# Performance work log

Measured on AMD Instinct MI355X. Metric: run time of the kernel, lower is better.

The kernel has to match this reference:

```python
import jax, jax.numpy as jnp
import numpy as np

B, S, N, F = 4, 8, 1024, 6
H, L, K, D = 64, 3, 16, 3  # hidden, layers, neighbors, num_dims
EPS = 1e-6


def setup_inputs() -> dict:
    key = jax.random.key(0)
    ks = iter(jax.random.split(key, 64))

    def w(shape, fan_in):
        return jax.random.normal(next(ks), shape, jnp.float32) / np.sqrt(fan_in)

    inp = {
        'points': jax.random.normal(next(ks), (B, S, N, F), jnp.float32),
        'w_in': w((F, H), F), 'b_in': jnp.zeros((H,), jnp.float32),
        # stacked per-layer params for the 3 PointTransformerLayers
        'Wq': w((L, H, H), H), 'bq': jnp.zeros((L, H), jnp.float32),
        'Wk': w((L, H, H), H), 'bk': jnp.zeros((L, H), jnp.float32),
        'Wv': w((L, H, H), H), 'bv': jnp.zeros((L, H), jnp.float32),
        'Wpe': w((L, D, H), D), 'bpe': jnp.zeros((L, H), jnp.float32),
        'Wpd': w((L, D, H), D), 'bpd': jnp.zeros((L, H), jnp.float32),
        'Wa': w((L, H, 1), H), 'ba': jnp.zeros((L, 1), jnp.float32),
        'Wo': w((L, H, H), H), 'bo': jnp.zeros((L, H), jnp.float32),
        'ln_s': jnp.ones((L, H), jnp.float32), 'ln_b': jnp.zeros((L, H), jnp.float32),
        # EncoderTransformerLayer params
        'Wek': w((H, H), H), 'bek': jnp.zeros((H,), jnp.float32),
        'Weq': w((H, H), H), 'beq': jnp.zeros((H,), jnp.float32),
        'Wev': w((H, H), H), 'bev': jnp.zeros((H,), jnp.float32),
        'We1': w((H, H), H), 'be1': jnp.zeros((H,), jnp.float32),
        'We2': w((H, H), H), 'be2': jnp.zeros((H,), jnp.float32),
        'ln2_s': jnp.ones((H,), jnp.float32), 'ln2_b': jnp.zeros((H,), jnp.float32),
    }
    return inp


def _layernorm(x, scale, bias):
    mu = jnp.mean(x, axis=-1, keepdims=True)
    var = jnp.var(x, axis=-1, keepdims=True)
    return (x - mu) * jax.lax.rsqrt(var + EPS) * scale + bias


def _point_layer(x, pos, Wq, bq, Wk, bk, Wv, bv, Wpe, bpe, Wpd, bpd, Wa, ba, Wo, bo):
    # x: [B,S,N,H], pos: [B,S,N,3]
    q = x @ Wq + bq
    k = x @ Wk + bk
    v = x @ Wv + bv
    pos_enc = pos @ Wpe + bpe  # [B,S,N,H]
    # pairwise squared distances: diff[i,j] = pos[i] - pos[j]
    pos_diff = pos[..., :, None, :] - pos[..., None, :, :]  # [B,S,N,N,3]
    dist = jnp.sum(pos_diff ** 2, axis=-1)                  # [B,S,N,N]
    _, nidx = jax.lax.top_k(-dist, K)                       # [B,S,N,K]

    def gather(a):  # a: [B,S,N,C] -> [B,S,N,K,C]
        return jnp.take_along_axis(a[:, :, None], nidx[..., None], axis=3)

    k_n = gather(k)
    v_n = gather(v)
    p_n = gather(pos_enc)
    qp = (q + pos_enc)[..., None, :]                        # [B,S,N,1,H]
    pd_enc = (gather(pos) - pos[..., None, :]) @ Wpd + bpd  # [B,S,N,K,H]
    scale = jnp.sqrt(jnp.float32(H))
    attn = qp * (k_n + p_n + pd_enc) / scale                # [B,S,N,K,H]
    attn = (attn @ Wa + ba).squeeze(-1)                     # [B,S,N,K]
    attn = jax.nn.softmax(attn, axis=-1)
    out = jnp.sum(attn[..., None] * v_n, axis=-2)           # [B,S,N,H]
    out = jax.nn.gelu(out @ Wo + bo)
    return x + out


def _encoder_layer(x, Wek, bek, Weq, beq, Wev, bev, We1, be1, We2, be2):
    k = x @ Wek + bek
    q = x @ Weq + beq
    v = x @ Wev + bev
    aw = jnp.einsum('bth,bsh->bts', q, k)
    aw = jax.nn.softmax(aw / jnp.sqrt(jnp.float32(H)), axis=-1)
    out = jnp.einsum('bts,bsh->bth', aw, v)
    out = jax.nn.gelu(out @ We1 + be1) @ We2 + be2
    return x + out


def reference(points, w_in, b_in, Wq, bq, Wk, bk, Wv, bv, Wpe, bpe, Wpd, bpd,
              Wa, ba, Wo, bo, ln_s, ln_b, Wek, bek, Weq, beq, Wev, bev,
              We1, be1, We2, be2, ln2_s, ln2_b):
    pos = points[..., :D]
    x = points @ w_in + b_in
    for i in range(L):
        x = _point_layer(x, pos, Wq[i], bq[i], Wk[i], bk[i], Wv[i], bv[i],
                         Wpe[i], bpe[i], Wpd[i], bpd[i], Wa[i], ba[i], Wo[i], bo[i])
        x = _layernorm(x, ln_s[i], ln_b[i])
    x = jnp.max(x, axis=-2)  # pool over points -> [B,S,H]
    x = _encoder_layer(x, Wek, bek, Weq, beq, Wev, bev, We1, be1, We2, be2)
    x = _layernorm(x, ln2_s, ln2_b)
    x = jnp.max(x, axis=-2)  # pool over seq -> [B,H]
    return x
```

## Files before the change

kernel.cpp:

```cpp
#include <hip/hip_runtime.h>
#include <cfloat>
#include <cmath>
#include <cstdint>

#define NPT   1024
#define NCL   32
#define PTOT  32768
#define HH    64
#define KNN_K 16
#define KNN_BLKS (NCL * 256)

#define RFL(x) __builtin_amdgcn_readfirstlane(x)

__device__ __forceinline__ float wave_sum64(float t) {
#pragma unroll
  for (int o = 32; o > 0; o >>= 1) t += __shfl_xor(t, o, 64);
  return t;
}

template <int NV>
__device__ __forceinline__ float mreduce(const float (&P)[NV], int lane) {
  float buf[NV];
#pragma unroll
  for (int i = 0; i < NV; ++i) buf[i] = P[i];
#pragma unroll
  for (int s = 0; (1 << s) < NV; ++s) {
    bool hi = (lane & (1 << s)) != 0;
#pragma unroll
    for (int m = 0; m < (NV >> (s + 1)); ++m) {
      float a = buf[2 * m], b = buf[2 * m + 1];
      float keep = hi ? b : a;
      float send = hi ? a : b;
      buf[m] = keep + __shfl_xor(send, 1 << s, 64);
    }
  }
  float t = buf[0];
#pragma unroll
  for (int o = NV; o < 64; o <<= 1) t += __shfl_xor(t, o, 64);
  return t;
}

__device__ __forceinline__ float gelu_f(float z) {
  float zc = 0.7978845608028654f * (z + 0.044715f * z * z * z);
  float t = __expf(2.0f * zc);
  float th = 1.0f - 2.0f / (t + 1.0f);
  return 0.5f * z * (1.0f + th);
}

__global__ __launch_bounds__(256) void k_front(
    const float* __restrict__ pts, const float* __restrict__ w_in,
    const float* __restrict__ b_in, float* __restrict__ x,
    float* __restrict__ pos4, int* __restrict__ nidx) {
  if (blockIdx.x >= KNN_BLKS) {
    int p = (blockIdx.x - KNN_BLKS) * 4 + (threadIdx.x >> 6);
    int h = threadIdx.x & 63;
    const float* pp = pts + p * 6;
    float acc = b_in[h];
#pragma unroll
    for (int f = 0; f < 6; ++f) acc += pp[f] * w_in[f * HH + h];
    x[p * HH + h] = acc;
    if (h < 4) pos4[p * 4 + h] = (h < 3) ? pp[h] : 0.0f;
    return;
  }

  __shared__ float sx[NPT], sy[NPT], sz[NPT];
  int cloud = blockIdx.x >> 8;
  int qbase = (blockIdx.x & 255) * 4;
  const float* cp = pts + (size_t)cloud * NPT * 6;
  for (int j = threadIdx.x; j < NPT; j += 256) {
    sx[j] = cp[j * 6 + 0];
    sy[j] = cp[j * 6 + 1];
    sz[j] = cp[j * 6 + 2];
  }
  __syncthreads();

  int wv = threadIdx.x >> 6;
  int lane = threadIdx.x & 63;
  int i = qbase + wv;
  float qx = sx[i], qy = sy[i], qz = sz[i];

  unsigned du[16];
#pragma unroll
  for (int c = 0; c < 16; ++c) {
    int j = c * 64 + lane;
    float dx = qx - sx[j], dy = qy - sy[j], dz = qz - sz[j];
    float d2 = __fadd_rn(__fadd_rn(__fmul_rn(dx, dx), __fmul_rn(dy, dy)),
                         __fmul_rn(dz, dz));
    du[c] = __float_as_uint(d2);
  }

  unsigned t = 0u;
#pragma unroll
  for (int bit = 30; bit >= 15; --bit) {
    unsigned tp = t | (1u << bit);
    int cnt = 0;
#pragma unroll
    for (int c = 0; c < 16; ++c)
      cnt += __popcll(__ballot(du[c] < tp));
    if (cnt <= 15) t = tp;
  }

  int obase = (cloud * NPT + i) * KNN_K;
  unsigned long long below = (1ull << lane) - 1ull;
  int slot = 0;
#pragma unroll
  for (int c = 0; c < 16; ++c) {
    bool lt = du[c] < t;
    unsigned long long m = __ballot(lt);
    if (lt) {
      int off = __popcll(m & below);
      nidx[obase + slot + off] = c * 64 + lane;
    }
    slot += __popcll(m);
  }

  int erem = KNN_K - slot;
  unsigned hi_end = t + (1u << 15);
  unsigned bu[16];
#pragma unroll
  for (int c = 0; c < 16; ++c)
    bu[c] = (du[c] >= t && du[c] < hi_end) ? du[c] : 0xFFFFFFFFu;
  for (int r2 = 0; r2 < erem; ++r2) {
    unsigned bd = bu[0];
    int bc = 0;
#pragma unroll
    for (int c = 1; c < 16; ++c) {
      if (bu[c] < bd) { bd = bu[c]; bc = c; }
    }
    unsigned gd = bd;
#pragma unroll
    for (int o = 32; o > 0; o >>= 1) {
      unsigned g2 = (unsigned)__shfl_xor((int)gd, o, 64);
      gd = (g2 < gd) ? g2 : gd;
    }
    int myidx = bc * 64 + lane;
    int gidx = (bd == gd) ? myidx : 0x7fffffff;
#pragma unroll
    for (int o = 32; o > 0; o >>= 1) {
      int g2 = __shfl_xor(gidx, o, 64);
      gidx = (g2 < gidx) ? g2 : gidx;
    }
    if (lane == 0) nidx[obase + slot + r2] = gidx;
    int sel = (myidx == gidx) ? bc : 99;
#pragma unroll
    for (int c = 0; c < 16; ++c) bu[c] = (c == sel) ? 0xFFFFFFFFu : bu[c];
  }
}

__global__ __launch_bounds__(256) void k_qkv_gemm(
    const float* __restrict__ x, const float* __restrict__ pos4,
    const float* __restrict__ Wq, const float* __restrict__ bq,
    const float* __restrict__ Wk, const float* __restrict__ bk,
    const float* __restrict__ Wv, const float* __restrict__ bv,
    const float* __restrict__ Wpe, const float* __restrict__ bpe,
    const float* __restrict__ Wpd, const float* __restrict__ bpd,
    float* __restrict__ qq, float* __restrict__ kkv) {
  int lane = threadIdx.x & 63;
  int pb = RFL(blockIdx.x * 16 + (threadIdx.x >> 6) * 4);
  const float* xw = x + (size_t)pb * HH;
  const float4* posw = reinterpret_cast<const float4*>(pos4) + pb;

  float wpe0 = Wpe[lane], wpe1 = Wpe[HH + lane], wpe2 = Wpe[2 * HH + lane];
  float wpd0 = Wpd[lane], wpd1 = Wpd[HH + lane], wpd2 = Wpd[2 * HH + lane];
  float we0 = wpe0 + wpd0, we1 = wpe1 + wpd1, we2 = wpe2 + wpd2;
  float bqq = bq[lane] + bpe[lane];
  float bkk = bk[lane] + bpe[lane] + bpd[lane];
  float bvv = bv[lane];

  float aq[4], ak[4], av[4];
#pragma unroll
  for (int p = 0; p < 4; ++p) { aq[p] = bqq; ak[p] = bkk; av[p] = bvv; }

#pragma unroll
  for (int c = 0; c < 8; ++c) {
    float wq8[8], wk8[8], wv8[8];
#pragma unroll
    for (int j = 0; j < 8; ++j) {
      int g = c * 8 + j;
      wq8[j] = Wq[g * HH + lane];
      wk8[j] = Wk[g * HH + lane];
      wv8[j] = Wv[g * HH + lane];
    }
#pragma unroll
    for (int p = 0; p < 4; ++p) {
#pragma unroll
      for (int j = 0; j < 8; ++j) {
        float xv = xw[p * HH + c * 8 + j];
        aq[p] = fmaf(xv, wq8[j], aq[p]);
        ak[p] = fmaf(xv, wk8[j], ak[p]);
        av[p] = fmaf(xv, wv8[j], av[p]);
      }
    }
  }

#pragma unroll
  for (int p = 0; p < 4; ++p) {
    float4 pp = posw[p];
    float qv = aq[p] + pp.x * wpe0 + pp.y * wpe1 + pp.z * wpe2;
    float kv = ak[p] + pp.x * we0 + pp.y * we1 + pp.z * we2;
    qq[(size_t)(pb + p) * HH + lane] = qv;
    reinterpret_cast<float2*>(kkv + ((size_t)(pb + p) << 7))[lane] =
        make_float2(kv, av[p]);
  }
}

__global__ __launch_bounds__(256) void k_attn_core(
    float* __restrict__ qq, const float* __restrict__ kkv,
    const int* __restrict__ nidx, const float* __restrict__ pos4,
    const float* __restrict__ Wpd, const float* __restrict__ Wa,
    const float* __restrict__ ba) {
  int lane = threadIdx.x & 63;
  int bid = blockIdx.x;
  int vb = (bid & 7) * (PTOT / 4 / 8) + (bid >> 3);
  int pu = RFL(vb * 4 + (threadIdx.x >> 6));
  int cbase = pu & ~(NPT - 1);

  float4 pp = reinterpret_cast<const float4*>(pos4)[pu];
  float u = qq[(size_t)pu * HH + lane] * Wa[lane] * 0.125f;
  float pdq = pp.x * Wpd[lane] + pp.y * Wpd[HH + lane] + pp.z * Wpd[2 * HH + lane];
  float C0 = wave_sum64(u * pdq) - ba[0];

  const int4* niw = reinterpret_cast<const int4*>(nidx + (size_t)pu * KNN_K);
  int nj[KNN_K];
#pragma unroll
  for (int g = 0; g < 4; ++g) {
    int4 r = niw[g];
    nj[g * 4 + 0] = r.x; nj[g * 4 + 1] = r.y;
    nj[g * 4 + 2] = r.z; nj[g * 4 + 3] = r.w;
  }

  float vj[KNN_K], P[KNN_K];
#pragma unroll
  for (int jj = 0; jj < KNN_K; ++jj) {
    float2 kv = reinterpret_cast<const float2*>(
        kkv + ((size_t)(cbase + nj[jj]) << 7))[lane];
    vj[jj] = kv.y;
    P[jj] = u * kv.x;
  }

  float T = mreduce<16>(P, lane);
  float lg = T - C0;

  float mx = lg;
#pragma unroll
  for (int o = 1; o < 16; o <<= 1) mx = fmaxf(mx, __shfl_xor(mx, o, 64));
  float e = __expf(lg - mx);
  float s = e;
#pragma unroll
  for (int o = 1; o < 16; o <<= 1) s += __shfl_xor(s, o, 64);

  float oacc = 0.f;
  int sb = lane & 48;
#pragma unroll
  for (int jj = 0; jj < KNN_K; ++jj)
    oacc = fmaf(__shfl(e, sb | jj, 64), vj[jj], oacc);

  qq[(size_t)pu * HH + lane] = oacc / s;
}

__global__ __launch_bounds__(256) void k_wo_ln(
    const float* __restrict__ outb, const float* __restrict__ Wo,
    const float* __restrict__ bo, float* __restrict__ x,
    const float* __restrict__ ln_s, const float* __restrict__ ln_b,
    float* __restrict__ partial, int do_pool) {
  __shared__ float red[4][HH];
  int lane = threadIdx.x & 63;
  int wv = threadIdx.x >> 6;
  int pb = RFL(blockIdx.x * 16 + wv * 4);
  const float* ow = outb + (size_t)pb * HH;

  float acc[4];
  float b0 = bo[lane];
#pragma unroll
  for (int p = 0; p < 4; ++p) acc[p] = b0;

#pragma unroll
  for (int c = 0; c < 8; ++c) {
    float w8[8];
#pragma unroll
    for (int j = 0; j < 8; ++j) w8[j] = Wo[(c * 8 + j) * HH + lane];
#pragma unroll
    for (int p = 0; p < 4; ++p) {
#pragma unroll
      for (int j = 0; j < 8; ++j) {
        float ov = ow[p * HH + c * 8 + j];
        acc[p] = fmaf(ov, w8[j], acc[p]);
      }
    }
  }

  float sg = ln_s[lane], bg = ln_b[lane];
  float xn[4];
#pragma unroll
  for (int p = 0; p < 4; ++p)
    xn[p] = x[(size_t)(pb + p) * HH + lane] + gelu_f(acc[p]);

  float Ts = mreduce<4>(xn, lane);
  float dd[4], sq[4];
#pragma unroll
  for (int p = 0; p < 4; ++p) {
    float mu = __shfl(Ts, p, 64) * (1.0f / HH);
    dd[p] = xn[p] - mu;
    sq[p] = dd[p] * dd[p];
  }
  float Tv = mreduce<4>(sq, lane);
  float mxp = -FLT_MAX;
#pragma unroll
  for (int p = 0; p < 4; ++p) {
    float var = __shfl(Tv, p, 64) * (1.0f / HH);
    float yv = dd[p] * rsqrtf(var + 1e-6f) * sg + bg;
    x[(size_t)(pb + p) * HH + lane] = yv;
    mxp = fmaxf(mxp, yv);
  }

  if (do_pool) {
    red[wv][lane] = mxp;
    __syncthreads();
    if (wv == 0) {
      float m = fmaxf(fmaxf(red[0][lane], red[1][lane]),
                      fmaxf(red[2][lane], red[3][lane]));
      partial[(size_t)blockIdx.x * HH + lane] = m;
    }
  }
}

__global__ __launch_bounds__(512) void k_enc(
    const float* __restrict__ partial,
    const float* __restrict__ Wek, const float* __restrict__ bek,
    const float* __restrict__ Weq, const float* __restrict__ beq,
    const float* __restrict__ Wev, const float* __restrict__ bev,
    const float* __restrict__ We1, const float* __restrict__ be1,
    const float* __restrict__ We2, const float* __restrict__ be2,
    const float* __restrict__ ln2_s, const float* __restrict__ ln2_b,
    float* __restrict__ out) {
  __shared__ float xs[8][HH], ks[8][HH], vs[8][HH], x2[8][HH];
  int b = blockIdx.x;
  int t = threadIdx.x >> 6;
  int h = threadIdx.x & 63;
  {
    int ci = b * 8 + t;
    const float* pp = partial + (size_t)ci * 64 * HH + h;
    float mx = pp[0];
#pragma unroll
    for (int c8 = 1; c8 < 64; ++c8) mx = fmaxf(mx, pp[c8 * HH]);
    xs[t][h] = mx;
  }
  __syncthreads();

  float kk = bek[h], qq = beq[h], vv = bev[h];
#pragma unroll 8
  for (int g = 0; g < HH; ++g) {
    float xv = xs[t][g];
    kk += xv * Wek[g * HH + h];
    qq += xv * Weq[g * HH + h];
    vv += xv * Wev[g * HH + h];
  }
  ks[t][h] = kk;
  vs[t][h] = vv;
  __syncthreads();

  float logit[8];
#pragma unroll
  for (int s = 0; s < 8; ++s) {
    float tt = qq * ks[s][h];
    logit[s] = wave_sum64(tt) * 0.125f;
  }
  float m = logit[0];
#pragma unroll
  for (int s = 1; s < 8; ++s) m = fmaxf(m, logit[s]);
  float ssum = 0.f;
#pragma unroll
  for (int s = 0; s < 8; ++s) { logit[s] = expf(logit[s] - m); ssum += logit[s]; }
  float o = 0.f;
#pragma unroll
  for (int s = 0; s < 8; ++s) o += (logit[s] / ssum) * vs[s][h];

  float h1 = be1[h];
#pragma unroll 8
  for (int g = 0; g < HH; ++g) h1 += __shfl(o, g, 64) * We1[g * HH + h];
  h1 = gelu_f(h1);
  float h2 = be2[h];
#pragma unroll 8
  for (int g = 0; g < HH; ++g) h2 += __shfl(h1, g, 64) * We2[g * HH + h];

  float xn = xs[t][h] + h2;
  float mu = wave_sum64(xn) * (1.0f / HH);
  float d = xn - mu;
  float var = wave_sum64(d * d) * (1.0f / HH);
  float yv = d * rsqrtf(var + 1e-6f) * ln2_s[h] + ln2_b[h];
  x2[t][h] = yv;
  __syncthreads();
  if (t == 0) {
    float mm = x2[0][h];
#pragma unroll
    for (int s = 1; s < 8; ++s) mm = fmaxf(mm, x2[s][h]);
    out[b * HH + h] = mm;
  }
}

extern "C" void kernel_launch(void* const* d_in, const int* in_sizes, int n_in,
                              void* d_out, int out_size, void* d_ws, size_t ws_size,
                              hipStream_t stream) {
  const float* points = (const float*)d_in[0];
  const float* w_in   = (const float*)d_in[1];
  const float* b_in   = (const float*)d_in[2];
  const float* Wq     = (const float*)d_in[3];
  const float* bq     = (const float*)d_in[4];
  const float* Wk     = (const float*)d_in[5];
  const float* bk     = (const float*)d_in[6];
  const float* Wv     = (const float*)d_in[7];
  const float* bv     = (const float*)d_in[8];
  const float* Wpe    = (const float*)d_in[9];
  const float* bpe    = (const float*)d_in[10];
  const float* Wpd    = (const float*)d_in[11];
  const float* bpd    = (const float*)d_in[12];
  const float* Wa     = (const float*)d_in[13];
  const float* ba     = (const float*)d_in[14];
  const float* Wo     = (const float*)d_in[15];
  const float* bo     = (const float*)d_in[16];
  const float* ln_s   = (const float*)d_in[17];
  const float* ln_b   = (const float*)d_in[18];
  const float* Wek    = (const float*)d_in[19];
  const float* bek    = (const float*)d_in[20];
  const float* Weq    = (const float*)d_in[21];
  const float* beq    = (const float*)d_in[22];
  const float* Wev    = (const float*)d_in[23];
  const float* bev    = (const float*)d_in[24];
  const float* We1    = (const float*)d_in[25];
  const float* be1    = (const float*)d_in[26];
  const float* We2    = (const float*)d_in[27];
  const float* be2    = (const float*)d_in[28];
  const float* ln2_s  = (const float*)d_in[29];
  const float* ln2_b  = (const float*)d_in[30];

  float* ws      = (float*)d_ws;
  float* pos4    = ws;
  float* xbuf    = pos4 + 4 * PTOT;
  float* qbuf    = xbuf + 64 * PTOT;
  float* kkv     = qbuf + 64 * PTOT;
  float* partial = kkv + 128 * PTOT;
  int*   nidx    = (int*)(partial + 2048 * HH);

  k_front<<<KNN_BLKS + PTOT / 4, 256, 0, stream>>>(points, w_in, b_in,
                                                   xbuf, pos4, nidx);

  for (int l = 0; l < 3; ++l) {
    k_qkv_gemm<<<PTOT / 16, 256, 0, stream>>>(xbuf, pos4,
        Wq + l * HH * HH, bq + l * HH,
        Wk + l * HH * HH, bk + l * HH,
        Wv + l * HH * HH, bv + l * HH,
        Wpe + l * 3 * HH, bpe + l * HH,
        Wpd + l * 3 * HH, bpd + l * HH,
        qbuf, kkv);
    k_attn_core<<<PTOT / 4, 256, 0, stream>>>(qbuf, kkv, nidx, pos4,
        Wpd + l * 3 * HH, Wa + l * HH, ba + l);
    k_wo_ln<<<PTOT / 16, 256, 0, stream>>>(qbuf,
        Wo + l * HH * HH, bo + l * HH, xbuf,
        ln_s + l * HH, ln_b + l * HH, partial, l == 2 ? 1 : 0);
  }

  k_enc<<<4, 512, 0, stream>>>(partial, Wek, bek, Weq, beq, Wev, bev,
                               We1, be1, We2, be2, ln2_s, ln2_b, (float*)d_out);
}
```

Baseline: 239.5 us.

## Fuse neighbor attention with Wo projection, GELU and layernorm kernel

```diff
diff --git a/kernel.cpp b/kernel.cpp
--- a/kernel.cpp
+++ b/kernel.cpp
@@ -204,70 +204,73 @@
   }
 }
 
-__global__ __launch_bounds__(256) void k_attn_core(
-    float* __restrict__ qq, const float* __restrict__ kkv,
+__global__ __launch_bounds__(256) void k_attn_wo(
+    const float* __restrict__ qq, const float* __restrict__ kkv,
     const int* __restrict__ nidx, const float* __restrict__ pos4,
     const float* __restrict__ Wpd, const float* __restrict__ Wa,
-    const float* __restrict__ ba) {
-  int lane = threadIdx.x & 63;
-  int bid = blockIdx.x;
-  int vb = (bid & 7) * (PTOT / 4 / 8) + (bid >> 3);
-  int pu = RFL(vb * 4 + (threadIdx.x >> 6));
-  int cbase = pu & ~(NPT - 1);
-
-  float4 pp = reinterpret_cast<const float4*>(pos4)[pu];
-  float u = qq[(size_t)pu * HH + lane] * Wa[lane] * 0.125f;
-  float pdq = pp.x * Wpd[lane] + pp.y * Wpd[HH + lane] + pp.z * Wpd[2 * HH + lane];
-  float C0 = wave_sum64(u * pdq) - ba[0];
-
-  const int4* niw = reinterpret_cast<const int4*>(nidx + (size_t)pu * KNN_K);
-  int nj[KNN_K];
-#pragma unroll
-  for (int g = 0; g < 4; ++g) {
-    int4 r = niw[g];
-    nj[g * 4 + 0] = r.x; nj[g * 4 + 1] = r.y;
-    nj[g * 4 + 2] = r.z; nj[g * 4 + 3] = r.w;
-  }
-
-  float vj[KNN_K], P[KNN_K];
-#pragma unroll
-  for (int jj = 0; jj < KNN_K; ++jj) {
-    float2 kv = reinterpret_cast<const float2*>(
-        kkv + ((size_t)(cbase + nj[jj]) << 7))[lane];
-    vj[jj] = kv.y;
-    P[jj] = u * kv.x;
-  }
-
-  float T = mreduce<16>(P, lane);
-  float lg = T - C0;
-
-  float mx = lg;
-#pragma unroll
-  for (int o = 1; o < 16; o <<= 1) mx = fmaxf(mx, __shfl_xor(mx, o, 64));
-  float e = __expf(lg - mx);
-  float s = e;
-#pragma unroll
-  for (int o = 1; o < 16; o <<= 1) s += __shfl_xor(s, o, 64);
-
-  float oacc = 0.f;
-  int sb = lane & 48;
-#pragma unroll
-  for (int jj = 0; jj < KNN_K; ++jj)
-    oacc = fmaf(__shfl(e, sb | jj, 64), vj[jj], oacc);
-
-  qq[(size_t)pu * HH + lane] = oacc / s;
-}
-
-__global__ __launch_bounds__(256) void k_wo_ln(
-    const float* __restrict__ outb, const float* __restrict__ Wo,
-    const float* __restrict__ bo, float* __restrict__ x,
+    const float* __restrict__ ba,
+    const float* __restrict__ Wo, const float* __restrict__ bo,
+    float* __restrict__ x,
     const float* __restrict__ ln_s, const float* __restrict__ ln_b,
     float* __restrict__ partial, int do_pool) {
   __shared__ float red[4][HH];
   int lane = threadIdx.x & 63;
   int wv = threadIdx.x >> 6;
-  int pb = RFL(blockIdx.x * 16 + wv * 4);
-  const float* ow = outb + (size_t)pb * HH;
+  int bid = blockIdx.x;
+  int vb = (bid & 7) * (2048 / 8) + (bid >> 3);
+  int pb = RFL(vb * 16 + wv * 4);
+  int cbase = pb & ~(NPT - 1);
+
+  float wa = Wa[lane];
+  float wpd0 = Wpd[lane], wpd1 = Wpd[HH + lane], wpd2 = Wpd[2 * HH + lane];
+  float ba0 = ba[0];
+
+  float out[4];
+#pragma unroll
+  for (int p = 0; p < 4; ++p) {
+    int pu = pb + p;
+    float4 pp = reinterpret_cast<const float4*>(pos4)[pu];
+    float u = qq[(size_t)pu * HH + lane] * wa * 0.125f;
+    float pdq = pp.x * wpd0 + pp.y * wpd1 + pp.z * wpd2;
+    float C0 = wave_sum64(u * pdq) - ba0;
+
+    const int4* niw = reinterpret_cast<const int4*>(nidx + (size_t)pu * KNN_K);
+    int nj[KNN_K];
+#pragma unroll
+    for (int g = 0; g < 4; ++g) {
+      int4 r = niw[g];
+      nj[g * 4 + 0] = r.x; nj[g * 4 + 1] = r.y;
+      nj[g * 4 + 2] = r.z; nj[g * 4 + 3] = r.w;
+    }
+
+    float vj[KNN_K], P[KNN_K];
+#pragma unroll
+    for (int jj = 0; jj < KNN_K; ++jj) {
+      float2 kv = reinterpret_cast<const float2*>(
+          kkv + ((size_t)(cbase + nj[jj]) << 7))[lane];
+      vj[jj] = kv.y;
+      P[jj] = u * kv.x;
+    }
+
+    float T = mreduce<16>(P, lane);
+    float lg = T - C0;
+
+    float mx = lg;
+#pragma unroll
+    for (int o = 1; o < 16; o <<= 1) mx = fmaxf(mx, __shfl_xor(mx, o, 64));
+    float e = __expf(lg - mx);
+    float s = e;
+#pragma unroll
+    for (int o = 1; o < 16; o <<= 1) s += __shfl_xor(s, o, 64);
+
+    float oacc = 0.f;
+    int sb = lane & 48;
+#pragma unroll
+    for (int jj = 0; jj < KNN_K; ++jj)
+      oacc = fmaf(__shfl(e, sb | jj, 64), vj[jj], oacc);
+
+    out[p] = oacc / s;
+  }
 
   float acc[4];
   float b0 = bo[lane];
@@ -283,8 +286,8 @@
     for (int p = 0; p < 4; ++p) {
 #pragma unroll
       for (int j = 0; j < 8; ++j) {
-        float ov = ow[p * HH + c * 8 + j];
-        acc[p] = fmaf(ov, w8[j], acc[p]);
+        float og = __shfl(out[p], c * 8 + j, 64);
+        acc[p] = fmaf(og, w8[j], acc[p]);
       }
     }
   }
@@ -319,7 +322,7 @@
     if (wv == 0) {
       float m = fmaxf(fmaxf(red[0][lane], red[1][lane]),
                       fmaxf(red[2][lane], red[3][lane]));
-      partial[(size_t)blockIdx.x * HH + lane] = m;
+      partial[(size_t)vb * HH + lane] = m;
     }
   }
 }
@@ -452,9 +455,8 @@
         Wpe + l * 3 * HH, bpe + l * HH,
         Wpd + l * 3 * HH, bpd + l * HH,
         qbuf, kkv);
-    k_attn_core<<<PTOT / 4, 256, 0, stream>>>(qbuf, kkv, nidx, pos4,
-        Wpd + l * 3 * HH, Wa + l * HH, ba + l);
-    k_wo_ln<<<PTOT / 16, 256, 0, stream>>>(qbuf,
+    k_attn_wo<<<PTOT / 16, 256, 0, stream>>>(qbuf, kkv, nidx, pos4,
+        Wpd + l * 3 * HH, Wa + l * HH, ba + l,
         Wo + l * HH * HH, bo + l * HH, xbuf,
         ln_s + l * HH, ln_b + l * HH, partial, l == 2 ? 1 : 0);
   }
```

Result: slower. 339.8 us (+41.9%).
